# Kernel tuning notes

Measured on AMD Instinct MI355X. Metric: run time of the kernel, lower is better.

## Reference

```python
import jax, jax.numpy as jnp
import numpy as np

B, S, D = 2, 2048, 1024
H = 16
KEY_DIM = 1024   # full projected dim; original scales by sqrt(key_dim), NOT head_dim
VAL_DIM = 1024
OUT_DIM = 1024


def setup_inputs() -> dict:
    key = jax.random.key(0)
    ks = jax.random.split(key, 11)
    s = 0.02
    return {
        "queries": jax.random.normal(ks[0], (B, S, D), jnp.float32),
        "keys": jax.random.normal(ks[1], (B, S, D), jnp.float32),
        "values": jax.random.normal(ks[2], (B, S, D), jnp.float32),
        "Wq": jax.random.normal(ks[3], (D, KEY_DIM), jnp.float32) * s,
        "bq": jnp.zeros((KEY_DIM,), jnp.float32),
        "Wk": jax.random.normal(ks[4], (D, KEY_DIM), jnp.float32) * s,
        "bk": jnp.zeros((KEY_DIM,), jnp.float32),
        "Wv": jax.random.normal(ks[5], (D, VAL_DIM), jnp.float32) * s,
        "bv": jnp.zeros((VAL_DIM,), jnp.float32),
        "Wo": jax.random.normal(ks[6], (KEY_DIM, OUT_DIM), jnp.float32) * s,
        "bo": jnp.zeros((OUT_DIM,), jnp.float32),
    }


def _split_heads(x):
    # [B, S, H*dh] -> [B, H, S, dh]
    b, s, _ = x.shape
    return x.reshape(b, s, H, -1).transpose(0, 2, 1, 3)


def reference(queries, keys, values, Wq, bq, Wk, bk, Wv, bv, Wo, bo):
    q = _split_heads(queries @ Wq + bq)   # [B,H,S,dk]
    k = _split_heads(keys @ Wk + bk)      # [B,H,S,dk]
    v = _split_heads(values @ Wv + bv)    # [B,H,S,dv]
    scale = jnp.sqrt(jnp.float32(KEY_DIM))  # full key_dim, as in the source
    scores = jnp.einsum('bhqd,bhkd->bhqk', q, k) / scale  # [B,H,S,S]
    # Source calls F.softmax with no dim; torch's legacy rule picks dim=1
    # (the heads axis) for a 4-D tensor. Reproduced faithfully.
    weights = jax.nn.softmax(scores, axis=1)
    o = jnp.einsum('bhqk,bhkd->bhqd', weights, v)          # [B,H,S,dv]
    o = o.transpose(0, 2, 1, 3).reshape(B, S, KEY_DIM)     # merge heads
    return o @ Wo + bo
```

## Files before the change

kernel.cpp:

```cpp
#include <hip/hip_runtime.h>


typedef unsigned short ushort;
typedef __attribute__((ext_vector_type(8))) short short8;
typedef __attribute__((ext_vector_type(4))) short short4v;
typedef __attribute__((ext_vector_type(4))) float f32x4;
typedef __attribute__((ext_vector_type(4))) float float4v;
typedef __attribute__((ext_vector_type(4))) unsigned int uint4v;
typedef __attribute__((ext_vector_type(2))) unsigned int uint2v;

#define MFMA32(a, b, c) __builtin_amdgcn_mfma_f32_16x16x32_bf16(a, b, c, 0, 0, 0)
#define MFMA16(a, b, c) __builtin_amdgcn_mfma_f32_16x16x16bf16_1k(a, b, c, 0, 0, 0)

#define VMCNT(N) asm volatile("s_waitcnt vmcnt(" #N ")" ::: "memory")
#define SCHEDBAR() __builtin_amdgcn_sched_barrier(0)

__device__ __forceinline__ ushort f2bf(float f) {
    unsigned u = __float_as_uint(f);
    u += 0x7fffu + ((u >> 16) & 1u);
    return (ushort)(u >> 16);
}
__device__ __forceinline__ ushort f2hf(float f) {
    union { _Float16 h; ushort u; } c;
    c.h = (_Float16)f;
    return c.u;
}
__device__ __forceinline__ float hf2f(ushort h) {
    union { ushort u; _Float16 h; } c;
    c.u = h;
    return (float)c.h;
}

__device__ __forceinline__ void gload16(const ushort* g, ushort* l) {
    __builtin_amdgcn_global_load_lds(
        (__attribute__((address_space(1))) void*)(unsigned long long)(g),
        (__attribute__((address_space(3))) void*)(l), 16, 0, 0);
}

__global__ __launch_bounds__(256) void convert_x_kernel(
    const float* __restrict__ q, const float* __restrict__ k,
    const float* __restrict__ v, ushort* __restrict__ out) {
    const size_t NPER = 4194304ull;
    size_t idx = ((size_t)blockIdx.x * 256 + threadIdx.x) * 8;
    const size_t stride = (size_t)gridDim.x * 256 * 8;
    for (; idx < 3 * NPER; idx += stride) {
        const float* src;
        size_t off;
        if (idx < NPER)          { src = q; off = idx; }
        else if (idx < 2 * NPER) { src = k; off = idx - NPER; }
        else                     { src = v; off = idx - 2 * NPER; }
        float4v a = *(const float4v*)(src + off);
        float4v b = *(const float4v*)(src + off + 4);
        union { ushort u[8]; uint4v v4; } pk;
        #pragma unroll
        for (int j = 0; j < 4; j++) { pk.u[j] = f2bf(a[j]); pk.u[4 + j] = f2bf(b[j]); }
        *(uint4v*)(out + idx) = pk.v4;
    }
}

__global__ __launch_bounds__(256) void transpose_w_kernel(
    const float* __restrict__ w0, const float* __restrict__ w1,
    const float* __restrict__ w2, const float* __restrict__ w3,
    ushort* __restrict__ Wt) {
    const float* W = blockIdx.z == 0 ? w0 : blockIdx.z == 1 ? w1 : blockIdx.z == 2 ? w2 : w3;
    ushort* out = Wt + (size_t)blockIdx.z * 1024 * 1024;
    __shared__ ushort st[64 * 72];
    int t = threadIdx.x;
    int kb = blockIdx.y * 64, nb = blockIdx.x * 64;
    int c4 = (t & 15) * 4;
    int r0 = t >> 4;
    #pragma unroll
    for (int p = 0; p < 4; p++) {
        int r = r0 + p * 16;
        float4v f = *(const float4v*)(W + (size_t)(kb + r) * 1024 + nb + c4);
        union { ushort u[4]; uint2v v2; } pk;
        #pragma unroll
        for (int j = 0; j < 4; j++) pk.u[j] = f2bf(f[j]);
        *(uint2v*)(st + r * 72 + c4) = pk.v2;
    }
    __syncthreads();
    int n = t >> 2;
    int kc = (t & 3) * 16;
    union { ushort u[16]; uint4v v4[2]; } tw;
    #pragma unroll
    for (int j = 0; j < 16; j++) tw.u[j] = st[(kc + j) * 72 + n];
    uint4v* dst = (uint4v*)(out + (size_t)(nb + n) * 1024 + kb + kc);
    dst[0] = tw.v4[0];
    dst[1] = tw.v4[1];
}

__device__ __forceinline__ void gemm_core(
    const ushort* __restrict__ A, const ushort* __restrict__ Bt,
    const float* __restrict__ bias, ushort* __restrict__ Cb,
    float* __restrict__ Cf, int mode, ushort* sA, ushort* sB) {
    int tid = threadIdx.x, lane = tid & 63, wave = tid >> 6;
    int li = lane & 15, g = lane >> 4;
    int mt = blockIdx.y * 128, nt = blockIdx.x * 128;
    int wm = (wave >> 1) * 64, wn = (wave & 1) * 64;
    f32x4 acc[4][4] = {};
    for (int k0 = 0; k0 < 1024; k0 += 64) {
        __syncthreads();
        #pragma unroll
        for (int i = 0; i < 4; i++) {
            int c = tid + i * 256;
            int row = c >> 3, chd = c & 7;
            int cg = chd ^ (row & 7);
            gload16(A + (size_t)(mt + row) * 1024 + k0 + cg * 8, sA + c * 8);
            gload16(Bt + (size_t)(nt + row) * 1024 + k0 + cg * 8, sB + c * 8);
        }
        __syncthreads();
        #pragma unroll
        for (int kk = 0; kk < 2; kk++) {
            short8 af[4], bfr[4];
            #pragma unroll
            for (int i = 0; i < 4; i++) {
                int ra = wm + i * 16 + li;
                int cb = kk * 64 + g * 16;
                af[i] = *(const short8*)((char*)sA + ra * 128 + (cb ^ ((ra & 7) << 4)));
                int rb = wn + i * 16 + li;
                bfr[i] = *(const short8*)((char*)sB + rb * 128 + (cb ^ ((rb & 7) << 4)));
            }
            #pragma unroll
            for (int mi = 0; mi < 4; mi++)
                #pragma unroll
                for (int ni = 0; ni < 4; ni++)
                    acc[mi][ni] = MFMA32(af[mi], bfr[ni], acc[mi][ni]);
        }
    }
    #pragma unroll
    for (int mi = 0; mi < 4; mi++) {
        #pragma unroll
        for (int ni = 0; ni < 4; ni++) {
            int n = nt + wn + ni * 16 + li;
            int m0 = mt + wm + mi * 16 + g * 4;
            float bv = bias[n];
            if (mode == 0) {
                #pragma unroll
                for (int r = 0; r < 4; r++)
                    Cb[(size_t)(m0 + r) * 1024 + n] = f2bf(acc[mi][ni][r] + bv);
            } else if (mode == 1) {
                int batch = m0 >> 11, mm = m0 & 2047;
                union { ushort u[4]; uint2v v2; } pk;
                #pragma unroll
                for (int r = 0; r < 4; r++) pk.u[r] = f2bf(acc[mi][ni][r] + bv);
                *(uint2v*)(Cb + (size_t)batch * 1024 * 2048 + (size_t)n * 2048 + mm) = pk.v2;
            } else {
                #pragma unroll
                for (int r = 0; r < 4; r++)
                    Cf[(size_t)(m0 + r) * 1024 + n] = acc[mi][ni][r] + bv;
            }
        }
    }
}

__global__ __launch_bounds__(256, 2) void proj_kernel(
    const ushort* __restrict__ Xb, const ushort* __restrict__ Wt,
    const float* __restrict__ bq, const float* __restrict__ bk,
    const float* __restrict__ bv, ushort* __restrict__ Qb,
    ushort* __restrict__ Kb, ushort* __restrict__ Vtb) {
    __shared__ ushort sA[128 * 64];
    __shared__ ushort sB[128 * 64];
    int z = blockIdx.z;
    const float* bias = z == 0 ? bq : (z == 1 ? bk : bv);
    ushort* out = z == 0 ? Qb : (z == 1 ? Kb : Vtb);
    gemm_core(Xb + (size_t)z * 4194304ull, Wt + (size_t)z * 1048576ull,
              bias, out, nullptr, z == 2 ? 1 : 0, sA, sB);
}

__global__ __launch_bounds__(256, 2) void outproj_kernel(
    const ushort* __restrict__ Ob, const ushort* __restrict__ Wt3,
    const float* __restrict__ bo, float* __restrict__ out) {
    __shared__ ushort sA[128 * 64];
    __shared__ ushort sB[128 * 64];
    gemm_core(Ob, Wt3, bo, nullptr, out, 2, sA, sB);
}

__global__ __launch_bounds__(256, 2) void zsum_kernel(
    const ushort* __restrict__ Qb, const ushort* __restrict__ Kb,
    ushort* __restrict__ Zln) {
    __shared__ ushort sQ[64 * 64];
    __shared__ ushort sK[128 * 64];
    int tid = threadIdx.x, lane = tid & 63, wid = tid >> 6;
    int li = lane & 15, g = lane >> 4;
    int bid = blockIdx.x;
    int swz = (bid & 7) * 128 + (bid >> 3);
    int qt = swz & 31, C = swz >> 5;
    int b = C >> 4, kg = C & 15;
    int q0 = qt * 64, k0 = kg * 128;
    const ushort* Qp = Qb + (size_t)(b * 2048 + q0) * 1024;
    const ushort* Kp = Kb + (size_t)(b * 2048 + k0) * 1024;
    f32x4 zacc[4][2] = {};
    for (int h = 0; h < 16; h++) {
        int co = h * 64;
        __syncthreads();
        #pragma unroll
        for (int i = 0; i < 2; i++) {
            int c = tid + i * 256;
            int r = c >> 3, m = c & 7;
            gload16(Qp + (size_t)r * 1024 + co + (m ^ (r & 7)) * 8, sQ + c * 8);
        }
        #pragma unroll
        for (int i = 0; i < 4; i++) {
            int c = tid + i * 256;
            int r = c >> 3, m = c & 7;
            gload16(Kp + (size_t)r * 1024 + co + (m ^ (r & 7)) * 8, sK + c * 8);
        }
        __syncthreads();
        short8 qf[4][2], kf[2][2];
        #pragma unroll
        for (int qs = 0; qs < 4; qs++)
            #pragma unroll
            for (int dc = 0; dc < 2; dc++) {
                int row = qs * 16 + li;
                qf[qs][dc] = *(const short8*)(
                    (char*)sQ + row * 128 + ((dc * 64 + g * 16) ^ ((row & 7) << 4)));
            }
        #pragma unroll
        for (int ks = 0; ks < 2; ks++)
            #pragma unroll
            for (int dc = 0; dc < 2; dc++) {
                int row = wid * 32 + ks * 16 + li;
                kf[ks][dc] = *(const short8*)(
                    (char*)sK + row * 128 + ((dc * 64 + g * 16) ^ ((row & 7) << 4)));
            }
        #pragma unroll
        for (int qs = 0; qs < 4; qs++)
            #pragma unroll
            for (int ks = 0; ks < 2; ks++) {
                f32x4 st = {0.f, 0.f, 0.f, 0.f};
                st = MFMA32(kf[ks][0], qf[qs][0], st);
                st = MFMA32(kf[ks][1], qf[qs][1], st);
                #pragma unroll
                for (int r = 0; r < 4; r++)
                    zacc[qs][ks][r] += __expf(st[r] * 0.03125f);
            }
    }
    #pragma unroll
    for (int qs = 0; qs < 4; qs++)
        #pragma unroll
        for (int ks = 0; ks < 2; ks++) {
            union { ushort u[4]; uint2v v; } pk;
            #pragma unroll
            for (int r = 0; r < 4; r++)
                pk.u[r] = f2hf(__logf(zacc[qs][ks][r]));
            *(uint2v*)(Zln + (size_t)(b * 2048 + q0 + qs * 16 + li) * 2048 +
                       k0 + wid * 32 + ks * 16 + g * 4) = pk.v;
        }
}

__global__ __launch_bounds__(256, 2) void pv_kernel(
    const ushort* __restrict__ Qb, const ushort* __restrict__ Kb,
    const ushort* __restrict__ Vt, const ushort* __restrict__ Zln,
    ushort* __restrict__ Ob) {
    __shared__ ushort S[4][2][5120];
    int tid = threadIdx.x, lane = tid & 63, wv = tid >> 6;
    int li = lane & 15, g = lane >> 4;
    int bid = blockIdx.x;
    int swz = (bid & 7) * 64 + (bid >> 3);
    int hp = swz & 3, p = swz >> 2;
    int b = p >> 6, qt = p & 63;
    int q0 = qt * 32;
    int head = hp * 4 + wv;
    short8 qf[2][2];
    #pragma unroll
    for (int qs = 0; qs < 2; qs++)
        #pragma unroll
        for (int dc = 0; dc < 2; dc++)
            qf[qs][dc] = *(const short8*)(
                Qb + (size_t)(b * 2048 + q0 + qs * 16 + li) * 1024 +
                head * 64 + dc * 32 + g * 8);
    f32x4 oacc[2][4] = {};
    const ushort* Ksrc[4];
    const ushort* Vsrc[4];
    const ushort* Zsrc[2];
    #pragma unroll
    for (int i = 0; i < 4; i++) {
        int c = lane + i * 64;
        int kr = c >> 3, km = c & 7;
        Ksrc[i] = Kb + (size_t)(b * 2048 + kr) * 1024 + head * 64 + (km ^ (kr & 7)) * 8;
        int vr = c >> 2, vm = c & 3;
        Vsrc[i] = Vt + (size_t)(b * 1024 + head * 64 + vr) * 2048 + (vm ^ ((vr >> 1) & 3)) * 8;
    }
    #pragma unroll
    for (int i = 0; i < 2; i++) {
        int c = lane + i * 64;
        int zr = c >> 2, zm = c & 3;
        Zsrc[i] = Zln + (size_t)(b * 2048 + q0 + zr) * 2048 + (zm ^ ((zr >> 1) & 3)) * 8;
    }
    #define PV_STAGE(BUF, KB)                                                  \
        {                                                                      \
            ushort* dst = S[wv][BUF];                                          \
            _Pragma("unroll") for (int i = 0; i < 4; i++)                      \
                gload16(Ksrc[i] + (size_t)(KB) * 1024, dst + (lane + i * 64) * 8); \
            _Pragma("unroll") for (int i = 0; i < 4; i++)                      \
                gload16(Vsrc[i] + (KB), dst + 2048 + (lane + i * 64) * 8);     \
            _Pragma("unroll") for (int i = 0; i < 2; i++)                      \
                gload16(Zsrc[i] + (KB), dst + 4096 + (lane + i * 64) * 8);     \
        }
    PV_STAGE(0, 0)
    for (int it = 0; it < 64; ++it) {
        int cur = it & 1;
        int kb = it * 32;
        if (it + 1 < 64) {
            PV_STAGE(cur ^ 1, kb + 32)
            VMCNT(10);
        } else {
            VMCNT(0);
        }
        SCHEDBAR();
        const char* Wb = (const char*)S[wv][cur];
        short8 kf[2][2];
        #pragma unroll
        for (int ks = 0; ks < 2; ks++)
            #pragma unroll
            for (int dc = 0; dc < 2; dc++) {
                int rk = ks * 16 + li;
                kf[ks][dc] = *(const short8*)(
                    Wb + rk * 128 + ((dc * 64 + g * 16) ^ ((rk & 7) << 4)));
            }
        short4v pf[2][2];
        #pragma unroll
        for (int qs = 0; qs < 2; qs++)
            #pragma unroll
            for (int ks = 0; ks < 2; ks++) {
                f32x4 st = {0.f, 0.f, 0.f, 0.f};
                st = MFMA32(kf[ks][0], qf[qs][0], st);
                st = MFMA32(kf[ks][1], qf[qs][1], st);
                int sl = ks * 4 + g;
                int rq = qs * 16 + li;
                union { ushort u[4]; uint2v v; } rz;
                rz.v = *(const uint2v*)(
                    Wb + 8192 + rq * 64 +
                    (((sl >> 1) ^ ((rq >> 1) & 3)) * 2 + (sl & 1)) * 8);
                float e0 = __expf(__builtin_fmaf(st[0], 0.03125f, -hf2f(rz.u[0])));
                float e1 = __expf(__builtin_fmaf(st[1], 0.03125f, -hf2f(rz.u[1])));
                float e2 = __expf(__builtin_fmaf(st[2], 0.03125f, -hf2f(rz.u[2])));
                float e3 = __expf(__builtin_fmaf(st[3], 0.03125f, -hf2f(rz.u[3])));
                unsigned a0 = __float_as_uint(e0) + 0x8000u;
                unsigned a1 = __float_as_uint(e1) + 0x8000u;
                unsigned a2 = __float_as_uint(e2) + 0x8000u;
                unsigned a3 = __float_as_uint(e3) + 0x8000u;
                union { unsigned u[2]; short4v s; } pk;
                pk.u[0] = __builtin_amdgcn_perm(a1, a0, 0x07060302u);
                pk.u[1] = __builtin_amdgcn_perm(a3, a2, 0x07060302u);
                pf[qs][ks] = pk.s;
            }
        #pragma unroll
        for (int ks = 0; ks < 2; ks++) {
            int sl = ks * 4 + g;
            #pragma unroll
            for (int ds = 0; ds < 4; ds++) {
                int rv = ds * 16 + li;
                short4v vf = *(const short4v*)(
                    Wb + 4096 + rv * 64 +
                    (((sl >> 1) ^ ((rv >> 1) & 3)) * 2 + (sl & 1)) * 8);
                oacc[0][ds] = MFMA16(pf[0][ks], vf, oacc[0][ds]);
                oacc[1][ds] = MFMA16(pf[1][ks], vf, oacc[1][ds]);
            }
        }
    }
    #undef PV_STAGE
    ushort* Oo = Ob + (size_t)(b * 2048 + q0) * 1024 + head * 64;
    #pragma unroll
    for (int qs = 0; qs < 2; qs++)
        #pragma unroll
        for (int ds = 0; ds < 4; ds++)
            #pragma unroll
            for (int r = 0; r < 4; r++)
                Oo[(size_t)(qs * 16 + g * 4 + r) * 1024 + ds * 16 + li] =
                    f2bf(oacc[qs][ds][r]);
}

extern "C" void kernel_launch(void* const* d_in, const int* in_sizes, int n_in,
                              void* d_out, int out_size, void* d_ws, size_t ws_size,
                              hipStream_t stream) {
    const float* queries = (const float*)d_in[0];
    const float* keys    = (const float*)d_in[1];
    const float* values  = (const float*)d_in[2];
    const float* Wq = (const float*)d_in[3];
    const float* bq = (const float*)d_in[4];
    const float* Wk = (const float*)d_in[5];
    const float* bk = (const float*)d_in[6];
    const float* Wv = (const float*)d_in[7];
    const float* bv = (const float*)d_in[8];
    const float* Wo = (const float*)d_in[9];
    const float* bo = (const float*)d_in[10];
    float* out = (float*)d_out;

    ushort* Xb  = (ushort*)d_ws;
    ushort* Wt  = Xb + 12ull * 1024 * 1024;
    ushort* Qb  = Wt + 4ull * 1024 * 1024;
    ushort* Kb  = Qb + 4ull * 1024 * 1024;
    ushort* Vtb = Kb + 4ull * 1024 * 1024;
    ushort* Zln = Xb;
    ushort* Ob  = Xb + 8ull * 1024 * 1024;

    convert_x_kernel<<<2048, 256, 0, stream>>>(queries, keys, values, Xb);
    transpose_w_kernel<<<dim3(16, 16, 4), 256, 0, stream>>>(Wq, Wk, Wv, Wo, Wt);
    proj_kernel<<<dim3(8, 32, 3), 256, 0, stream>>>(Xb, Wt, bq, bk, bv, Qb, Kb, Vtb);
    zsum_kernel<<<1024, 256, 0, stream>>>(Qb, Kb, Zln);
    pv_kernel<<<512, 256, 0, stream>>>(Qb, Kb, Vtb, Zln, Ob);
    outproj_kernel<<<dim3(8, 32), 256, 0, stream>>>(Ob, Wt + 3ull * 1024 * 1024, bo, out);
}
```

Measured before the change: 181.7 us.

## Split pv_kernel key range across wave pairs and reduce partial outputs via LDS

Each head is now handled by two waves, each covering half of the 2048 keys, with per-iteration key chunks halved to 16 and LDS staging halved. The partial output accumulators are summed through shared memory after a block barrier, and only the odd wave writes the result. The grid doubles to 1024 blocks and launch bounds raise occupancy to 4 blocks per CU, aiming at better latency hiding and load balance. In exchange each iteration does less work per wait, and the kernel adds a reduction step and a barrier at the end.

Measured after the change: 229.4 us. 1.26x slower.

```diff
diff --git a/kernel.cpp b/kernel.cpp
--- a/kernel.cpp
+++ b/kernel.cpp
@@ -248,19 +248,20 @@
         }
 }
 
-__global__ __launch_bounds__(256, 2) void pv_kernel(
+__global__ __launch_bounds__(256, 4) void pv_kernel(
     const ushort* __restrict__ Qb, const ushort* __restrict__ Kb,
     const ushort* __restrict__ Vt, const ushort* __restrict__ Zln,
     ushort* __restrict__ Ob) {
-    __shared__ ushort S[4][2][5120];
+    __shared__ ushort S[4][2][2560];
     int tid = threadIdx.x, lane = tid & 63, wv = tid >> 6;
     int li = lane & 15, g = lane >> 4;
     int bid = blockIdx.x;
-    int swz = (bid & 7) * 64 + (bid >> 3);
-    int hp = swz & 3, p = swz >> 2;
-    int b = p >> 6, qt = p & 63;
+    int swz = (bid & 7) * 128 + (bid >> 3);
+    int hp2 = swz & 7, pp = swz >> 3;
+    int b = pp >> 6, qt = pp & 63;
     int q0 = qt * 32;
-    int head = hp * 4 + wv;
+    int head = hp2 * 2 + (wv >> 1);
+    int kseg = (wv & 1) * 1024;
     short8 qf[2][2];
     #pragma unroll
     for (int qs = 0; qs < 2; qs++)
@@ -270,105 +271,111 @@
                 Qb + (size_t)(b * 2048 + q0 + qs * 16 + li) * 1024 +
                 head * 64 + dc * 32 + g * 8);
     f32x4 oacc[2][4] = {};
-    const ushort* Ksrc[4];
-    const ushort* Vsrc[4];
-    const ushort* Zsrc[2];
-    #pragma unroll
-    for (int i = 0; i < 4; i++) {
+    const ushort* Ksrc[2];
+    const ushort* Vsrc[2];
+    const ushort* Zsrc;
+    #pragma unroll
+    for (int i = 0; i < 2; i++) {
         int c = lane + i * 64;
         int kr = c >> 3, km = c & 7;
-        Ksrc[i] = Kb + (size_t)(b * 2048 + kr) * 1024 + head * 64 + (km ^ (kr & 7)) * 8;
-        int vr = c >> 2, vm = c & 3;
-        Vsrc[i] = Vt + (size_t)(b * 1024 + head * 64 + vr) * 2048 + (vm ^ ((vr >> 1) & 3)) * 8;
-    }
-    #pragma unroll
-    for (int i = 0; i < 2; i++) {
-        int c = lane + i * 64;
-        int zr = c >> 2, zm = c & 3;
-        Zsrc[i] = Zln + (size_t)(b * 2048 + q0 + zr) * 2048 + (zm ^ ((zr >> 1) & 3)) * 8;
+        Ksrc[i] = Kb + (size_t)(b * 2048 + kseg + kr) * 1024 + head * 64 +
+                  (km ^ (kr & 7)) * 8;
+        int vr = c >> 1, vm = c & 1;
+        Vsrc[i] = Vt + (size_t)(b * 1024 + head * 64 + vr) * 2048 + kseg +
+                  (vm ^ ((vr >> 1) & 1)) * 8;
+    }
+    {
+        int zr = lane >> 1, zm = lane & 1;
+        Zsrc = Zln + (size_t)(b * 2048 + q0 + zr) * 2048 + kseg +
+               (zm ^ ((zr >> 1) & 1)) * 8;
     }
     #define PV_STAGE(BUF, KB)                                                  \
         {                                                                      \
             ushort* dst = S[wv][BUF];                                          \
-            _Pragma("unroll") for (int i = 0; i < 4; i++)                      \
-                gload16(Ksrc[i] + (size_t)(KB) * 1024, dst + (lane + i * 64) * 8); \
-            _Pragma("unroll") for (int i = 0; i < 4; i++)                      \
-                gload16(Vsrc[i] + (KB), dst + 2048 + (lane + i * 64) * 8);     \
-            _Pragma("unroll") for (int i = 0; i < 2; i++)                      \
-                gload16(Zsrc[i] + (KB), dst + 4096 + (lane + i * 64) * 8);     \
+            gload16(Ksrc[0] + (size_t)(KB) * 1024, dst + lane * 8);            \
+            gload16(Ksrc[1] + (size_t)(KB) * 1024, dst + (lane + 64) * 8);     \
+            gload16(Vsrc[0] + (KB), dst + 1024 + lane * 8);                    \
+            gload16(Vsrc[1] + (KB), dst + 1024 + (lane + 64) * 8);             \
+            gload16(Zsrc + (KB), dst + 2048 + lane * 8);                       \
         }
     PV_STAGE(0, 0)
     for (int it = 0; it < 64; ++it) {
         int cur = it & 1;
-        int kb = it * 32;
         if (it + 1 < 64) {
-            PV_STAGE(cur ^ 1, kb + 32)
-            VMCNT(10);
+            PV_STAGE(cur ^ 1, (it + 1) * 16)
+            VMCNT(5);
         } else {
             VMCNT(0);
         }
         SCHEDBAR();
         const char* Wb = (const char*)S[wv][cur];
-        short8 kf[2][2];
-        #pragma unroll
-        for (int ks = 0; ks < 2; ks++)
-            #pragma unroll
-            for (int dc = 0; dc < 2; dc++) {
-                int rk = ks * 16 + li;
-                kf[ks][dc] = *(const short8*)(
-                    Wb + rk * 128 + ((dc * 64 + g * 16) ^ ((rk & 7) << 4)));
-            }
-        short4v pf[2][2];
+        short8 kf0 = *(const short8*)(Wb + li * 128 + ((g * 16) ^ ((li & 7) << 4)));
+        short8 kf1 = *(const short8*)(Wb + li * 128 + ((64 + g * 16) ^ ((li & 7) << 4)));
+        short4v pf[2];
+        #pragma unroll
+        for (int qs = 0; qs < 2; qs++) {
+            f32x4 st = {0.f, 0.f, 0.f, 0.f};
+            st = MFMA32(kf0, qf[qs][0], st);
+            st = MFMA32(kf1, qf[qs][1], st);
+            int rq = qs * 16 + li;
+            union { ushort u[4]; uint2v v; } rz;
+            rz.v = *(const uint2v*)(
+                Wb + 4096 + rq * 32 +
+                (((g >> 1) ^ ((rq >> 1) & 1)) * 2 + (g & 1)) * 8);
+            float e0 = __expf(__builtin_fmaf(st[0], 0.03125f, -hf2f(rz.u[0])));
+            float e1 = __expf(__builtin_fmaf(st[1], 0.03125f, -hf2f(rz.u[1])));
+            float e2 = __expf(__builtin_fmaf(st[2], 0.03125f, -hf2f(rz.u[2])));
+            float e3 = __expf(__builtin_fmaf(st[3], 0.03125f, -hf2f(rz.u[3])));
+            unsigned a0 = __float_as_uint(e0) + 0x8000u;
+            unsigned a1 = __float_as_uint(e1) + 0x8000u;
+            unsigned a2 = __float_as_uint(e2) + 0x8000u;
+            unsigned a3 = __float_as_uint(e3) + 0x8000u;
+            union { unsigned u[2]; short4v s; } pk;
+            pk.u[0] = __builtin_amdgcn_perm(a1, a0, 0x07060302u);
+            pk.u[1] = __builtin_amdgcn_perm(a3, a2, 0x07060302u);
+            pf[qs] = pk.s;
+        }
+        #pragma unroll
+        for (int ds = 0; ds < 4; ds++) {
+            int rv = ds * 16 + li;
+            short4v vf = *(const short4v*)(
+                Wb + 2048 + rv * 32 +
+                (((g >> 1) ^ ((rv >> 1) & 1)) * 2 + (g & 1)) * 8);
+            oacc[0][ds] = MFMA16(pf[0], vf, oacc[0][ds]);
+            oacc[1][ds] = MFMA16(pf[1], vf, oacc[1][ds]);
+        }
+    }
+    #undef PV_STAGE
+    if ((wv & 1) == 0) {
+        float* ex = (float*)(&S[wv][0][0]);
         #pragma unroll
         for (int qs = 0; qs < 2; qs++)
             #pragma unroll
-            for (int ks = 0; ks < 2; ks++) {
-                f32x4 st = {0.f, 0.f, 0.f, 0.f};
-                st = MFMA32(kf[ks][0], qf[qs][0], st);
-                st = MFMA32(kf[ks][1], qf[qs][1], st);
-                int sl = ks * 4 + g;
-                int rq = qs * 16 + li;
-                union { ushort u[4]; uint2v v; } rz;
-                rz.v = *(const uint2v*)(
-                    Wb + 8192 + rq * 64 +
-                    (((sl >> 1) ^ ((rq >> 1) & 3)) * 2 + (sl & 1)) * 8);
-                float e0 = __expf(__builtin_fmaf(st[0], 0.03125f, -hf2f(rz.u[0])));
-                float e1 = __expf(__builtin_fmaf(st[1], 0.03125f, -hf2f(rz.u[1])));
-                float e2 = __expf(__builtin_fmaf(st[2], 0.03125f, -hf2f(rz.u[2])));
-                float e3 = __expf(__builtin_fmaf(st[3], 0.03125f, -hf2f(rz.u[3])));
-                unsigned a0 = __float_as_uint(e0) + 0x8000u;
-                unsigned a1 = __float_as_uint(e1) + 0x8000u;
-                unsigned a2 = __float_as_uint(e2) + 0x8000u;
-                unsigned a3 = __float_as_uint(e3) + 0x8000u;
-                union { unsigned u[2]; short4v s; } pk;
-                pk.u[0] = __builtin_amdgcn_perm(a1, a0, 0x07060302u);
-                pk.u[1] = __builtin_amdgcn_perm(a3, a2, 0x07060302u);
-                pf[qs][ks] = pk.s;
-            }
-        #pragma unroll
-        for (int ks = 0; ks < 2; ks++) {
-            int sl = ks * 4 + g;
-            #pragma unroll
-            for (int ds = 0; ds < 4; ds++) {
-                int rv = ds * 16 + li;
-                short4v vf = *(const short4v*)(
-                    Wb + 4096 + rv * 64 +
-                    (((sl >> 1) ^ ((rv >> 1) & 3)) * 2 + (sl & 1)) * 8);
-                oacc[0][ds] = MFMA16(pf[0][ks], vf, oacc[0][ds]);
-                oacc[1][ds] = MFMA16(pf[1][ks], vf, oacc[1][ds]);
-            }
-        }
-    }
-    #undef PV_STAGE
-    ushort* Oo = Ob + (size_t)(b * 2048 + q0) * 1024 + head * 64;
-    #pragma unroll
-    for (int qs = 0; qs < 2; qs++)
-        #pragma unroll
-        for (int ds = 0; ds < 4; ds++)
-            #pragma unroll
-            for (int r = 0; r < 4; r++)
-                Oo[(size_t)(qs * 16 + g * 4 + r) * 1024 + ds * 16 + li] =
-                    f2bf(oacc[qs][ds][r]);
+            for (int ds = 0; ds < 4; ds++)
+                #pragma unroll
+                for (int r = 0; r < 4; r++)
+                    ex[((qs * 4 + ds) * 4 + r) * 64 + lane] = oacc[qs][ds][r];
+    }
+    __syncthreads();
+    if (wv & 1) {
+        const float* ex = (const float*)(&S[wv ^ 1][0][0]);
+        #pragma unroll
+        for (int qs = 0; qs < 2; qs++)
+            #pragma unroll
+            for (int ds = 0; ds < 4; ds++)
+                #pragma unroll
+                for (int r = 0; r < 4; r++)
+                    oacc[qs][ds][r] += ex[((qs * 4 + ds) * 4 + r) * 64 + lane];
+        ushort* Oo = Ob + (size_t)(b * 2048 + q0) * 1024 + head * 64;
+        #pragma unroll
+        for (int qs = 0; qs < 2; qs++)
+            #pragma unroll
+            for (int ds = 0; ds < 4; ds++)
+                #pragma unroll
+                for (int r = 0; r < 4; r++)
+                    Oo[(size_t)(qs * 16 + g * 4 + r) * 1024 + ds * 16 + li] =
+                        f2bf(oacc[qs][ds][r]);
+    }
 }
 
 extern "C" void kernel_launch(void* const* d_in, const int* in_sizes, int n_in,
@@ -399,6 +406,6 @@
     transpose_w_kernel<<<dim3(16, 16, 4), 256, 0, stream>>>(Wq, Wk, Wv, Wo, Wt);
     proj_kernel<<<dim3(8, 32, 3), 256, 0, stream>>>(Xb, Wt, bq, bk, bv, Qb, Kb, Vtb);
     zsum_kernel<<<1024, 256, 0, stream>>>(Qb, Kb, Zln);
-    pv_kernel<<<512, 256, 0, stream>>>(Qb, Kb, Vtb, Zln, Ob);
+    pv_kernel<<<1024, 256, 0, stream>>>(Qb, Kb, Vtb, Zln, Ob);
     outproj_kernel<<<dim3(8, 32), 256, 0, stream>>>(Ob, Wt + 3ull * 1024 * 1024, bo, out);
 }
```
